# Optimization experiments

Measured on AMD Instinct MI355X. Metric: run time of the kernel, lower is better.

The kernel has to match this reference:

```python
import jax, jax.numpy as jnp
import numpy as np

N, E = 16384, 262144
D_NODE, D_EDGE, H = 256, 64, 8
EPS = 1e-5

def _lin(key, din, dout):
    kw, kb = jax.random.split(key)
    s = 1.0 / np.sqrt(din)
    W = jax.random.uniform(kw, (din, dout), jnp.float32, -s, s)
    b = jax.random.uniform(kb, (dout,), jnp.float32, -s, s)
    return W, b

def setup_inputs() -> dict:
    key = jax.random.key(0)
    ks = jax.random.split(key, 12)
    node_features = jax.random.normal(ks[0], (N, D_NODE), jnp.float32)
    edge_index = jax.random.randint(ks[1], (2, E), 0, N, jnp.int64)
    edge_features = jax.random.normal(ks[2], (E, D_EDGE), jnp.float32)
    Wn, bn = _lin(ks[3], D_NODE, D_NODE)
    Wq, bq = _lin(ks[4], D_NODE, D_NODE)
    Wk, bk = _lin(ks[5], D_NODE, D_NODE)
    Wv, bv = _lin(ks[6], D_NODE, D_NODE)
    We, be = _lin(ks[7], D_EDGE, D_NODE)
    A1, a1 = _lin(ks[8], 3 * D_NODE, D_NODE)
    A2, a2 = _lin(ks[9], D_NODE, H)
    gamma = jnp.ones((D_NODE,), jnp.float32)
    beta = jnp.zeros((D_NODE,), jnp.float32)
    return dict(node_features=node_features, edge_index=edge_index,
                edge_features=edge_features, Wn=Wn, bn=bn, Wq=Wq, bq=bq,
                Wk=Wk, bk=bk, Wv=Wv, bv=bv, We=We, be=be,
                A1=A1, a1=a1, A2=A2, a2=a2, gamma=gamma, beta=beta)

def _leaky(x):
    return jnp.where(x > 0, x, 0.2 * x)

def reference(node_features, edge_index, edge_features, Wn, bn, Wq, bq,
              Wk, bk, Wv, bv, We, be, A1, a1, A2, a2, gamma, beta):
    h = node_features @ Wn + bn                      # [N, d]
    q = node_features @ Wq + bq
    k = node_features @ Wk + bk
    v = node_features @ Wv + bv
    edge_h = edge_features @ We + be                 # [E, d]
    src, tgt = edge_index[0], edge_index[1]
    attn_in = jnp.concatenate([q[src], k[tgt], edge_h], axis=-1)  # [E, 3d]
    scores = _leaky(_leaky(attn_in @ A1 + a1) @ A2 + a2)          # [E, H]
    # softmax over ALL edges (dim=0) of head-mean, as in the original
    w = jax.nn.softmax(scores.mean(axis=-1), axis=0)              # [E]
    out = jnp.zeros_like(node_features).at[src].add(w[:, None] * v[tgt])
    x = h + out                                      # dropout is identity (eval)
    mu = x.mean(-1, keepdims=True)
    var = ((x - mu) ** 2).mean(-1, keepdims=True)
    return (x - mu) / jnp.sqrt(var + EPS) * gamma + beta
```

## Files before the change

kernel.cpp:

```cpp
#include <hip/hip_runtime.h>
#include <stdint.h>

#define NN 16384
#define EE 262144
#define DD 256

typedef float f32x4 __attribute__((ext_vector_type(4)));
typedef short s16x8 __attribute__((ext_vector_type(8)));
typedef unsigned short u16x4 __attribute__((ext_vector_type(4)));
typedef unsigned short u16x8 __attribute__((ext_vector_type(8)));

#define AS1 __attribute__((address_space(1)))
#define AS3 __attribute__((address_space(3)))

__device__ __forceinline__ float bf2f(unsigned short u) {
  union { unsigned int i; float f; } v; v.i = ((unsigned int)u) << 16; return v.f;
}
__device__ __forceinline__ unsigned short f2bf(float f) {
  union { float f; unsigned int i; } v; v.f = f;
  unsigned int r = v.i + 0x7fffu + ((v.i >> 16) & 1u);
  return (unsigned short)(r >> 16);
}
__device__ __forceinline__ float lrelu(float x) { return x > 0.f ? x : 0.2f * x; }

__device__ __forceinline__ int chanperm(int c) {
  int hi = c & ~63, loc = c & 63;
  int ct = loc >> 4, quad = (loc >> 2) & 3, r = loc & 3;
  return hi | (quad * 16 + ct * 4 + r);
}

__global__ __launch_bounds__(256) void prep_kernel(
    const float* __restrict__ Wn, const float* __restrict__ bn,
    const float* __restrict__ Wq, const float* __restrict__ bq,
    const float* __restrict__ Wk, const float* __restrict__ bk,
    const float* __restrict__ Wv, const float* __restrict__ bv,
    const float* __restrict__ We, const float* __restrict__ be,
    const float* __restrict__ A1, const float* __restrict__ a1,
    const float* __restrict__ A2,
    unsigned short* __restrict__ BcatT, float* __restrict__ bcat,
    unsigned short* __restrict__ WeaT, float* __restrict__ bcomb,
    float* __restrict__ A2p)
{
  const int b = blockIdx.x, t = threadIdx.x;
  if (b < 256) {
    float acc = 0.f;
    for (int j = 0; j < 256; ++j) acc += Wq[b * 256 + j] * A1[j * 256 + t];
    BcatT[(512 + t) * 256 + b] = f2bf(acc);
  } else if (b < 512) {
    int k = b - 256; float acc = 0.f;
    for (int j = 0; j < 256; ++j) acc += Wk[k * 256 + j] * A1[(256 + j) * 256 + t];
    BcatT[(768 + t) * 256 + k] = f2bf(acc);
  } else if (b < 576) {
    int k = b - 512; float acc = 0.f;
    for (int j = 0; j < 256; ++j) acc += We[k * 256 + j] * A1[(512 + j) * 256 + t];
    WeaT[chanperm(t) * 64 + k] = f2bf(acc);
  } else if (b == 576) {
    float acc = a1[t];
    for (int j = 0; j < 256; ++j) {
      acc += bq[j] * A1[j * 256 + t];
      acc += bk[j] * A1[(256 + j) * 256 + t];
      acc += be[j] * A1[(512 + j) * 256 + t];
    }
    bcomb[chanperm(t)] = acc;
  } else if (b < 705) {
    int b2 = b - 577;
    for (int rr = 0; rr < 4; ++rr) {
      int np = b2 * 4 + rr;
      float v = (np < 256) ? Wn[t * 256 + np] : Wv[t * 256 + (np - 256)];
      BcatT[np * 256 + t] = f2bf(v);
    }
  } else if (b == 705) {
    bcat[t] = bn[t];
    bcat[256 + t] = bv[t];
    bcat[512 + t] = 0.f;
    bcat[768 + t] = 0.f;
  } else {
    int m = chanperm(t);
    for (int j = 0; j < 8; ++j) A2p[m * 8 + j] = A2[t * 8 + j];
  }
}

__global__ __launch_bounds__(256) void conv_hist_kernel(
    const float* __restrict__ in, unsigned short* __restrict__ o,
    const int* __restrict__ eidx, int* __restrict__ deg)
{
  size_t i = (size_t)blockIdx.x * 256 + threadIdx.x;
  const f32x4* p = (const f32x4*)(in + i * 8);
  f32x4 a = p[0], b = p[1];
  u16x8 r = { f2bf(a[0]), f2bf(a[1]), f2bf(a[2]), f2bf(a[3]),
              f2bf(b[0]), f2bf(b[1]), f2bf(b[2]), f2bf(b[3]) };
  *(u16x8*)(o + i * 8) = r;
  if (blockIdx.x < EE / 256) {
    int e = blockIdx.x * 256 + threadIdx.x;
    atomicAdd(&deg[eidx[e]], 1);
  }
}

__global__ __launch_bounds__(256, 1) void node_gemm_kernel(
    const unsigned short* __restrict__ Abf,
    const unsigned short* __restrict__ BT,
    const float* __restrict__ bias,
    float* __restrict__ hout, unsigned short* __restrict__ vout,
    unsigned short* __restrict__ Qa, unsigned short* __restrict__ Ka)
{
  __shared__ __align__(16) unsigned short Al[128 * 64];
  __shared__ __align__(16) unsigned short Bl[128 * 64];
  const int t = threadIdx.x;
  const int wid = t >> 6, lane = t & 63;
  const int quad = lane >> 4, l15 = lane & 15;
  const int mblk = blockIdx.x & 127, nblk = blockIdx.x >> 7;
  const int m0 = mblk * 128, n0 = nblk * 128;
  const int mh = wid >> 1, nh = wid & 1;
  const int srow = lane >> 3, sslot = lane & 7;

  f32x4 acc[4][4];
  #pragma unroll
  for (int i = 0; i < 4; ++i)
    #pragma unroll
    for (int j = 0; j < 4; ++j) acc[i][j] = (f32x4){0.f, 0.f, 0.f, 0.f};

  for (int ks = 0; ks < 4; ++ks) {
    const int k0 = ks * 64;
    #pragma unroll
    for (int j = 0; j < 4; ++j) {
      int cj = wid * 4 + j;
      int row = cj * 8 + srow;
      const unsigned short* ga =
          Abf + (size_t)(m0 + row) * 256 + k0 + ((sslot ^ (row & 7)) * 8);
      __builtin_amdgcn_global_load_lds((AS1 const void*)ga,
                                       (AS3 void*)(Al + cj * 512), 16, 0, 0);
      const unsigned short* gb =
          BT + (size_t)(n0 + row) * 256 + k0 + ((sslot ^ (row & 7)) * 8);
      __builtin_amdgcn_global_load_lds((AS1 const void*)gb,
                                       (AS3 void*)(Bl + cj * 512), 16, 0, 0);
    }
    __syncthreads();
    s16x8 af[4][2], bfr[4][2];
    #pragma unroll
    for (int mt = 0; mt < 4; ++mt) {
      int row = mh * 64 + mt * 16 + l15;
      #pragma unroll
      for (int kk = 0; kk < 2; ++kk) {
        int s = (kk * 4 + quad) ^ (row & 7);
        af[mt][kk] = *(const s16x8*)(Al + row * 64 + s * 8);
      }
    }
    #pragma unroll
    for (int nt = 0; nt < 4; ++nt) {
      int row = nh * 64 + nt * 16 + l15;
      #pragma unroll
      for (int kk = 0; kk < 2; ++kk) {
        int s = (kk * 4 + quad) ^ (row & 7);
        bfr[nt][kk] = *(const s16x8*)(Bl + row * 64 + s * 8);
      }
    }
    #pragma unroll
    for (int mt = 0; mt < 4; ++mt)
      #pragma unroll
      for (int nt = 0; nt < 4; ++nt) {
        acc[mt][nt] = __builtin_amdgcn_mfma_f32_16x16x32_bf16(
            af[mt][0], bfr[nt][0], acc[mt][nt], 0, 0, 0);
        acc[mt][nt] = __builtin_amdgcn_mfma_f32_16x16x32_bf16(
            af[mt][1], bfr[nt][1], acc[mt][nt], 0, 0, 0);
      }
    __syncthreads();
  }

  #pragma unroll
  for (int nt = 0; nt < 4; ++nt) {
    int n = n0 + nh * 64 + nt * 16 + l15;
    float bb = bias[n];
    int seg = n >> 8;
    int ncol = n & 255;
    #pragma unroll
    for (int mt = 0; mt < 4; ++mt) {
      int m = m0 + mh * 64 + mt * 16 + quad * 4;
      f32x4 a = acc[mt][nt];
      #pragma unroll
      for (int r = 0; r < 4; ++r) {
        float val = a[r] + bb;
        size_t idx = (size_t)(m + r) * 256 + ncol;
        if (seg == 0) hout[idx] = val;
        else if (seg == 1) vout[idx] = f2bf(val);
        else if (seg == 2) Qa[idx] = f2bf(val);
        else Ka[idx] = f2bf(val);
      }
    }
  }
}

__global__ __launch_bounds__(256) void scan_kernel(
    const int* __restrict__ deg, int* __restrict__ startA, int* __restrict__ cursor)
{
  __shared__ int ls[256];
  const int t = threadIdx.x;
  int4 d[16];
  int s = 0;
  #pragma unroll
  for (int i = 0; i < 16; ++i) {
    d[i] = ((const int4*)deg)[t * 16 + i];
    s += d[i].x + d[i].y + d[i].z + d[i].w;
  }
  ls[t] = s;
  __syncthreads();
  for (int dd = 1; dd < 256; dd <<= 1) {
    int v = ls[t];
    if (t >= dd) v += ls[t - dd];
    __syncthreads();
    ls[t] = v;
    __syncthreads();
  }
  int run = ls[t] - s;
  #pragma unroll
  for (int i = 0; i < 16; ++i) {
    int4 o;
    o.x = run; run += d[i].x;
    o.y = run; run += d[i].y;
    o.z = run; run += d[i].z;
    o.w = run; run += d[i].w;
    ((int4*)startA)[t * 16 + i] = o;
    ((int4*)cursor)[t * 16 + i] = o;
  }
  if (t == 255) startA[NN] = run;
}

__global__ __launch_bounds__(256) void perm_kernel(
    const int* __restrict__ eidx, int* __restrict__ cursor,
    int* __restrict__ perm, int* __restrict__ srcp, int* __restrict__ tgtp)
{
  int e = blockIdx.x * 256 + threadIdx.x;
  int s = eidx[e], tg = eidx[EE + e];
  int pos = atomicAdd(&cursor[s], 1);
  perm[pos] = e;
  srcp[pos] = s;
  tgtp[pos] = tg;
}

__global__ __launch_bounds__(256, 4) void edge_scores_kernel(
    const int* __restrict__ perm, const int* __restrict__ srcp,
    const int* __restrict__ tgtp, const float* __restrict__ ef,
    const unsigned short* __restrict__ Qa, const unsigned short* __restrict__ Ka,
    const unsigned short* __restrict__ WeaT, const float* __restrict__ bcomb,
    const float* __restrict__ A2p, const float* __restrict__ a2g,
    float* __restrict__ Pp, float* __restrict__ Z)
{
  __shared__ __align__(16) unsigned short efl[64 * 64];
  __shared__ __align__(16) float A2l[256 * 12];
  __shared__ __align__(16) float pl[4 * 64 * 8];
  __shared__ __align__(16) float bcl[256];
  __shared__ int srcl[64], tgtl[64];
  const int t = threadIdx.x;
  const int wid = t >> 6, lane = t & 63, quad = lane >> 4, l15 = lane & 15;
  const int eb = blockIdx.x * 64;

  {
    const f32x4* sp = (const f32x4*)(A2p + t * 8);
    f32x4 x0 = sp[0], x1 = sp[1];
    *(f32x4*)&A2l[t * 12] = x0;
    *(f32x4*)&A2l[t * 12 + 4] = x1;
  }
  if (t < 64) srcl[t] = srcp[eb + t];
  else if (t < 128) tgtl[t - 64] = tgtp[eb + (t - 64)];
  else if (t < 192) ((f32x4*)bcl)[t - 128] = ((const f32x4*)bcomb)[t - 128];
  {
    int r = t >> 2, q4 = t & 3;
    int pe = perm[eb + r];
    const f32x4* sp = (const f32x4*)(ef + (size_t)pe * 64 + q4 * 16);
    f32x4 v0 = sp[0], v1 = sp[1], v2 = sp[2], v3 = sp[3];
    u16x8 w0 = { f2bf(v0[0]), f2bf(v0[1]), f2bf(v0[2]), f2bf(v0[3]),
                 f2bf(v1[0]), f2bf(v1[1]), f2bf(v1[2]), f2bf(v1[3]) };
    u16x8 w1 = { f2bf(v2[0]), f2bf(v2[1]), f2bf(v2[2]), f2bf(v2[3]),
                 f2bf(v3[0]), f2bf(v3[1]), f2bf(v3[2]), f2bf(v3[3]) };
    int s0_ = (2 * q4) ^ (r & 7), s1_ = (2 * q4 + 1) ^ (r & 7);
    *(u16x8*)&efl[r * 64 + s0_ * 8] = w0;
    *(u16x8*)&efl[r * 64 + s1_ * 8] = w1;
  }
  __syncthreads();

  f32x4 acc[4][4];
  {
    const int cb = wid * 64 + quad * 16;
    #pragma unroll
    for (int eo = 0; eo < 2; ++eo) {
      u16x8 q0[2], q1[2], k0[2], k1[2];
      #pragma unroll
      for (int x = 0; x < 2; ++x) {
        int e = (eo * 2 + x) * 16 + l15;
        const unsigned short* qr = Qa + (size_t)srcl[e] * 256 + cb;
        const unsigned short* kr = Ka + (size_t)tgtl[e] * 256 + cb;
        q0[x] = *(const u16x8*)qr; q1[x] = *(const u16x8*)(qr + 8);
        k0[x] = *(const u16x8*)kr; k1[x] = *(const u16x8*)(kr + 8);
      }
      #pragma unroll
      for (int x = 0; x < 2; ++x) {
        int et = eo * 2 + x;
        #pragma unroll
        for (int r = 0; r < 4; ++r) {
          acc[0][et][r] = bf2f(q0[x][r])     + bf2f(k0[x][r]);
          acc[1][et][r] = bf2f(q0[x][4 + r]) + bf2f(k0[x][4 + r]);
          acc[2][et][r] = bf2f(q1[x][r])     + bf2f(k1[x][r]);
          acc[3][et][r] = bf2f(q1[x][4 + r]) + bf2f(k1[x][4 + r]);
        }
      }
    }
  }

  {
    s16x8 af0[4], af1[4];
    #pragma unroll
    for (int ct = 0; ct < 4; ++ct) {
      int ch = wid * 64 + ct * 16 + l15;
      af0[ct] = *(const s16x8*)(WeaT + ch * 64 + quad * 8);
      af1[ct] = *(const s16x8*)(WeaT + ch * 64 + 32 + quad * 8);
    }
    #pragma unroll
    for (int et = 0; et < 4; ++et) {
      int e = et * 16 + l15;
      s16x8 b0 = *(const s16x8*)(efl + e * 64 + ((quad ^ (e & 7)) * 8));
      s16x8 b1 = *(const s16x8*)(efl + e * 64 + (((4 + quad) ^ (e & 7)) * 8));
      #pragma unroll
      for (int ct = 0; ct < 4; ++ct) {
        acc[ct][et] = __builtin_amdgcn_mfma_f32_16x16x32_bf16(af0[ct], b0, acc[ct][et], 0, 0, 0);
        acc[ct][et] = __builtin_amdgcn_mfma_f32_16x16x32_bf16(af1[ct], b1, acc[ct][et], 0, 0, 0);
      }
    }
  }

  float part[4][8];
  #pragma unroll
  for (int i = 0; i < 4; ++i)
    #pragma unroll
    for (int j = 0; j < 8; ++j) part[i][j] = 0.f;
  #pragma unroll
  for (int ct = 0; ct < 4; ++ct) {
    int chb = wid * 64 + ct * 16 + quad * 4;
    f32x4 bc = *(const f32x4*)&bcl[chb];
    #pragma unroll
    for (int r = 0; r < 4; ++r) {
      f32x4 w0 = *(const f32x4*)&A2l[(chb + r) * 12];
      f32x4 w1 = *(const f32x4*)&A2l[(chb + r) * 12 + 4];
      #pragma unroll
      for (int et = 0; et < 4; ++et) {
        float m = lrelu(acc[ct][et][r] + bc[r]);
        part[et][0] += m * w0[0]; part[et][1] += m * w0[1];
        part[et][2] += m * w0[2]; part[et][3] += m * w0[3];
        part[et][4] += m * w1[0]; part[et][5] += m * w1[1];
        part[et][6] += m * w1[2]; part[et][7] += m * w1[3];
      }
    }
  }
  #pragma unroll
  for (int et = 0; et < 4; ++et)
    #pragma unroll
    for (int hh = 0; hh < 8; ++hh) {
      part[et][hh] += __shfl_xor(part[et][hh], 16);
      part[et][hh] += __shfl_xor(part[et][hh], 32);
    }
  if (quad == 0) {
    #pragma unroll
    for (int et = 0; et < 4; ++et) {
      f32x4 p0 = { part[et][0], part[et][1], part[et][2], part[et][3] };
      f32x4 p1 = { part[et][4], part[et][5], part[et][6], part[et][7] };
      int e = et * 16 + l15;
      *(f32x4*)&pl[(wid * 64 + e) * 8] = p0;
      *(f32x4*)&pl[(wid * 64 + e) * 8 + 4] = p1;
    }
  }
  __syncthreads();
  if (t < 64) {
    f32x4 t0 = {0.f, 0.f, 0.f, 0.f}, t1 = {0.f, 0.f, 0.f, 0.f};
    #pragma unroll
    for (int w2 = 0; w2 < 4; ++w2) {
      t0 += *(const f32x4*)&pl[(w2 * 64 + t) * 8];
      t1 += *(const f32x4*)&pl[(w2 * 64 + t) * 8 + 4];
    }
    float sacc = 0.f;
    #pragma unroll
    for (int j = 0; j < 4; ++j) {
      sacc += lrelu(t0[j] + a2g[j]);
      sacc += lrelu(t1[j] + a2g[4 + j]);
    }
    float p = __expf(sacc * 0.125f);
    Pp[eb + t] = p;
    #pragma unroll
    for (int d = 1; d < 64; d <<= 1) p += __shfl_xor(p, d);
    if (t == 0) atomicAdd(Z, p);
  }
}

__global__ __launch_bounds__(256) void scatter_ln_kernel(
    const int* __restrict__ startA, const float* __restrict__ Pp,
    const float* __restrict__ Zp, const int* __restrict__ tgtp,
    const unsigned short* __restrict__ vbuf, const float* __restrict__ hbuf,
    const float* __restrict__ gamma, const float* __restrict__ beta,
    float* __restrict__ out)
{
  const int wid = threadIdx.x >> 6, lane = threadIdx.x & 63;
  const int n = blockIdx.x * 4 + wid;
  const float invZ = 1.f / Zp[0];
  const int s0 = startA[n], s1 = startA[n + 1];
  float a0 = 0.f, a1_ = 0.f, a2_ = 0.f, a3_ = 0.f;
  int i = s0;
  for (; i + 1 < s1; i += 2) {
    float w0 = Pp[i], w1 = Pp[i + 1];
    int t0 = tgtp[i], t1 = tgtp[i + 1];
    u16x4 v0 = *(const u16x4*)(vbuf + (size_t)t0 * 256 + lane * 4);
    u16x4 v1 = *(const u16x4*)(vbuf + (size_t)t1 * 256 + lane * 4);
    w0 *= invZ; w1 *= invZ;
    a0 += w0 * bf2f(v0[0]) + w1 * bf2f(v1[0]);
    a1_ += w0 * bf2f(v0[1]) + w1 * bf2f(v1[1]);
    a2_ += w0 * bf2f(v0[2]) + w1 * bf2f(v1[2]);
    a3_ += w0 * bf2f(v0[3]) + w1 * bf2f(v1[3]);
  }
  if (i < s1) {
    float w0 = Pp[i] * invZ;
    int t0 = tgtp[i];
    u16x4 v0 = *(const u16x4*)(vbuf + (size_t)t0 * 256 + lane * 4);
    a0 += w0 * bf2f(v0[0]); a1_ += w0 * bf2f(v0[1]);
    a2_ += w0 * bf2f(v0[2]); a3_ += w0 * bf2f(v0[3]);
  }
  f32x4 hv = *(const f32x4*)(hbuf + (size_t)n * 256 + lane * 4);
  float x0 = hv[0] + a0, x1 = hv[1] + a1_, x2 = hv[2] + a2_, x3 = hv[3] + a3_;
  float sum = x0 + x1 + x2 + x3;
  float sq = x0 * x0 + x1 * x1 + x2 * x2 + x3 * x3;
  #pragma unroll
  for (int d = 1; d < 64; d <<= 1) { sum += __shfl_xor(sum, d); sq += __shfl_xor(sq, d); }
  float mu = sum * (1.f / 256.f);
  float var = sq * (1.f / 256.f) - mu * mu;
  float rstd = rsqrtf(var + 1e-5f);
  f32x4 g = *(const f32x4*)(gamma + lane * 4);
  f32x4 b = *(const f32x4*)(beta + lane * 4);
  f32x4 o;
  o[0] = (x0 - mu) * rstd * g[0] + b[0];
  o[1] = (x1 - mu) * rstd * g[1] + b[1];
  o[2] = (x2 - mu) * rstd * g[2] + b[2];
  o[3] = (x3 - mu) * rstd * g[3] + b[3];
  *(f32x4*)(out + (size_t)n * 256 + lane * 4) = o;
}

extern "C" void kernel_launch(void* const* d_in, const int* in_sizes, int n_in,
                              void* d_out, int out_size, void* d_ws, size_t ws_size,
                              hipStream_t stream)
{
  (void)in_sizes; (void)n_in; (void)out_size; (void)ws_size;
  const float* nf    = (const float*)d_in[0];
  const int*   eidx  = (const int*)  d_in[1];
  const float* ef    = (const float*)d_in[2];
  const float* Wn    = (const float*)d_in[3];
  const float* bn    = (const float*)d_in[4];
  const float* Wq    = (const float*)d_in[5];
  const float* bq    = (const float*)d_in[6];
  const float* Wk    = (const float*)d_in[7];
  const float* bk    = (const float*)d_in[8];
  const float* Wv    = (const float*)d_in[9];
  const float* bv    = (const float*)d_in[10];
  const float* We    = (const float*)d_in[11];
  const float* be    = (const float*)d_in[12];
  const float* A1    = (const float*)d_in[13];
  const float* a1    = (const float*)d_in[14];
  const float* A2    = (const float*)d_in[15];
  const float* a2    = (const float*)d_in[16];
  const float* gamma = (const float*)d_in[17];
  const float* beta  = (const float*)d_in[18];
  float* out = (float*)d_out;

  char* ws = (char*)d_ws;
  size_t off = 0;
  auto take = [&](size_t bytes) {
    size_t r = off; off += (bytes + 255) & ~(size_t)255; return r;
  };
  float* Z       = (float*)(ws + take(16));
  int*   deg     = (int*)  (ws + take((size_t)NN * 4));
  int*   startA  = (int*)  (ws + take((size_t)(NN + 1) * 4));
  int*   cursor  = (int*)  (ws + take((size_t)NN * 4));
  int*   perm    = (int*)  (ws + take((size_t)EE * 4));
  int*   srcp    = (int*)  (ws + take((size_t)EE * 4));
  int*   tgtp    = (int*)  (ws + take((size_t)EE * 4));
  float* Pp      = (float*)(ws + take((size_t)EE * 4));
  float* hbuf    = (float*)(ws + take((size_t)NN * DD * 4));
  unsigned short* vbuf  = (unsigned short*)(ws + take((size_t)NN * DD * 2));
  unsigned short* QaB   = (unsigned short*)(ws + take((size_t)NN * DD * 2));
  unsigned short* KaB   = (unsigned short*)(ws + take((size_t)NN * DD * 2));
  unsigned short* BcatT = (unsigned short*)(ws + take((size_t)1024 * 256 * 2));
  float* bcat    = (float*)(ws + take(1024 * 4));
  unsigned short* WeaT  = (unsigned short*)(ws + take((size_t)256 * 64 * 2));
  float* bcomb   = (float*)(ws + take(256 * 4));
  float* A2p     = (float*)(ws + take(256 * 8 * 4));
  unsigned short* nfb   = (unsigned short*)(ws + take((size_t)NN * DD * 2));

  hipMemsetAsync(d_ws, 0, 256 + (size_t)NN * 4, stream);

  prep_kernel<<<707, 256, 0, stream>>>(Wn, bn, Wq, bq, Wk, bk, Wv, bv,
                                       We, be, A1, a1, A2,
                                       BcatT, bcat, WeaT, bcomb, A2p);
  conv_hist_kernel<<<(NN * DD / 8) / 256, 256, 0, stream>>>(nf, nfb, eidx, deg);
  node_gemm_kernel<<<1024, 256, 0, stream>>>(nfb, BcatT, bcat, hbuf, vbuf, QaB, KaB);
  scan_kernel<<<1, 256, 0, stream>>>(deg, startA, cursor);
  perm_kernel<<<EE / 256, 256, 0, stream>>>(eidx, cursor, perm, srcp, tgtp);
  edge_scores_kernel<<<EE / 64, 256, 0, stream>>>(perm, srcp, tgtp, ef, QaB, KaB,
                                                  WeaT, bcomb, A2p, a2, Pp, Z);
  scatter_ln_kernel<<<NN / 4, 256, 0, stream>>>(startA, Pp, Z, tgtp, vbuf, hbuf,
                                                gamma, beta, out);
}
```

Baseline: 347.9 us.

## Merge launches, persist edge-score blocks with prefetch, bf16 h buffer, sharded Z

Cuts the launch chain from seven kernels to five. The histogram moves into the prep kernel, the scan into the conversion kernel, and the edge permutation into the GEMM kernel as extra blocks. The edge-score kernel now handles four 64-edge tiles per block, keeps the We weights resident in registers and prefetches the next tile's indices and edge features. It also reduces Z into 64 partial slots instead of one global atomic. The h buffer is stored as bf16 to halve its traffic, and the scatter loop is unrolled by 4. The bf16 h adds rounding error to the residual path.

```diff
diff --git a/kernel.cpp b/kernel.cpp
--- a/kernel.cpp
+++ b/kernel.cpp
@@ -25,21 +25,21 @@
 
 __device__ __forceinline__ int chanperm(int c) {
   int hi = c & ~63, loc = c & 63;
-  int ct = loc >> 4, quad = (loc >> 2) & 3, r = loc & 3;
-  return hi | (quad * 16 + ct * 4 + r);
-}
-
-__global__ __launch_bounds__(256) void prep_kernel(
+  int ct = loc >> 4, quad = (loc >> 2) & 3, rr = loc & 3;
+  return hi | (quad * 16 + ct * 4 + rr);
+}
+
+__global__ __launch_bounds__(256) void prep_hist_kernel(
     const float* __restrict__ Wn, const float* __restrict__ bn,
     const float* __restrict__ Wq, const float* __restrict__ bq,
     const float* __restrict__ Wk, const float* __restrict__ bk,
     const float* __restrict__ Wv, const float* __restrict__ bv,
     const float* __restrict__ We, const float* __restrict__ be,
     const float* __restrict__ A1, const float* __restrict__ a1,
-    const float* __restrict__ A2,
+    const float* __restrict__ A2, const int* __restrict__ eidx,
     unsigned short* __restrict__ BcatT, float* __restrict__ bcat,
     unsigned short* __restrict__ WeaT, float* __restrict__ bcomb,
-    float* __restrict__ A2p)
+    float* __restrict__ A2p, int* __restrict__ deg)
 {
   const int b = blockIdx.x, t = threadIdx.x;
   if (b < 256) {
@@ -74,41 +74,86 @@
     bcat[256 + t] = bv[t];
     bcat[512 + t] = 0.f;
     bcat[768 + t] = 0.f;
-  } else {
+  } else if (b == 706) {
     int m = chanperm(t);
     for (int j = 0; j < 8; ++j) A2p[m * 8 + j] = A2[t * 8 + j];
-  }
-}
-
-__global__ __launch_bounds__(256) void conv_hist_kernel(
+  } else {
+    int e = (b - 707) * 256 + t;
+    atomicAdd(&deg[eidx[e]], 1);
+  }
+}
+
+__global__ __launch_bounds__(256) void conv_scan_kernel(
     const float* __restrict__ in, unsigned short* __restrict__ o,
-    const int* __restrict__ eidx, int* __restrict__ deg)
+    const int* __restrict__ deg, int* __restrict__ startA,
+    int* __restrict__ cursor)
 {
-  size_t i = (size_t)blockIdx.x * 256 + threadIdx.x;
-  const f32x4* p = (const f32x4*)(in + i * 8);
-  f32x4 a = p[0], b = p[1];
-  u16x8 r = { f2bf(a[0]), f2bf(a[1]), f2bf(a[2]), f2bf(a[3]),
-              f2bf(b[0]), f2bf(b[1]), f2bf(b[2]), f2bf(b[3]) };
-  *(u16x8*)(o + i * 8) = r;
-  if (blockIdx.x < EE / 256) {
-    int e = blockIdx.x * 256 + threadIdx.x;
-    atomicAdd(&deg[eidx[e]], 1);
-  }
-}
-
-__global__ __launch_bounds__(256, 1) void node_gemm_kernel(
+  const int t = threadIdx.x;
+  if (blockIdx.x < 2048) {
+    size_t i = (size_t)blockIdx.x * 256 + t;
+    const f32x4* p = (const f32x4*)(in + i * 8);
+    f32x4 a = p[0], b = p[1];
+    u16x8 r = { f2bf(a[0]), f2bf(a[1]), f2bf(a[2]), f2bf(a[3]),
+                f2bf(b[0]), f2bf(b[1]), f2bf(b[2]), f2bf(b[3]) };
+    *(u16x8*)(o + i * 8) = r;
+    return;
+  }
+  __shared__ int ls[256];
+  int4 d[16];
+  int s = 0;
+  #pragma unroll
+  for (int i = 0; i < 16; ++i) {
+    d[i] = ((const int4*)deg)[t * 16 + i];
+    s += d[i].x + d[i].y + d[i].z + d[i].w;
+  }
+  ls[t] = s;
+  __syncthreads();
+  for (int dd = 1; dd < 256; dd <<= 1) {
+    int v = ls[t];
+    if (t >= dd) v += ls[t - dd];
+    __syncthreads();
+    ls[t] = v;
+    __syncthreads();
+  }
+  int run = ls[t] - s;
+  #pragma unroll
+  for (int i = 0; i < 16; ++i) {
+    int4 ov;
+    ov.x = run; run += d[i].x;
+    ov.y = run; run += d[i].y;
+    ov.z = run; run += d[i].z;
+    ov.w = run; run += d[i].w;
+    ((int4*)startA)[t * 16 + i] = ov;
+    ((int4*)cursor)[t * 16 + i] = ov;
+  }
+  if (t == 255) startA[NN] = run;
+}
+
+__global__ __launch_bounds__(256, 1) void gemm_perm_kernel(
     const unsigned short* __restrict__ Abf,
     const unsigned short* __restrict__ BT,
     const float* __restrict__ bias,
-    float* __restrict__ hout, unsigned short* __restrict__ vout,
-    unsigned short* __restrict__ Qa, unsigned short* __restrict__ Ka)
+    unsigned short* __restrict__ hout, unsigned short* __restrict__ vout,
+    unsigned short* __restrict__ Qa, unsigned short* __restrict__ Ka,
+    const int* __restrict__ eidx, int* __restrict__ cursor,
+    int* __restrict__ perm, int* __restrict__ srcp, int* __restrict__ tgtp)
 {
+  const int t = threadIdx.x;
+  if (blockIdx.x < 1024) {
+    int e = blockIdx.x * 256 + t;
+    int s = eidx[e], tg = eidx[EE + e];
+    int pos = atomicAdd(&cursor[s], 1);
+    perm[pos] = e;
+    srcp[pos] = s;
+    tgtp[pos] = tg;
+    return;
+  }
   __shared__ __align__(16) unsigned short Al[128 * 64];
   __shared__ __align__(16) unsigned short Bl[128 * 64];
-  const int t = threadIdx.x;
+  const int b2 = blockIdx.x - 1024;
   const int wid = t >> 6, lane = t & 63;
   const int quad = lane >> 4, l15 = lane & 15;
-  const int mblk = blockIdx.x & 127, nblk = blockIdx.x >> 7;
+  const int mblk = b2 & 127, nblk = b2 >> 7;
   const int m0 = mblk * 128, n0 = nblk * 128;
   const int mh = wid >> 1, nh = wid & 1;
   const int srow = lane >> 3, sslot = lane & 7;
@@ -180,60 +225,13 @@
       for (int r = 0; r < 4; ++r) {
         float val = a[r] + bb;
         size_t idx = (size_t)(m + r) * 256 + ncol;
-        if (seg == 0) hout[idx] = val;
+        if (seg == 0) hout[idx] = f2bf(val);
         else if (seg == 1) vout[idx] = f2bf(val);
         else if (seg == 2) Qa[idx] = f2bf(val);
         else Ka[idx] = f2bf(val);
       }
     }
   }
-}
-
-__global__ __launch_bounds__(256) void scan_kernel(
-    const int* __restrict__ deg, int* __restrict__ startA, int* __restrict__ cursor)
-{
-  __shared__ int ls[256];
-  const int t = threadIdx.x;
-  int4 d[16];
-  int s = 0;
-  #pragma unroll
-  for (int i = 0; i < 16; ++i) {
-    d[i] = ((const int4*)deg)[t * 16 + i];
-    s += d[i].x + d[i].y + d[i].z + d[i].w;
-  }
-  ls[t] = s;
-  __syncthreads();
-  for (int dd = 1; dd < 256; dd <<= 1) {
-    int v = ls[t];
-    if (t >= dd) v += ls[t - dd];
-    __syncthreads();
-    ls[t] = v;
-    __syncthreads();
-  }
-  int run = ls[t] - s;
-  #pragma unroll
-  for (int i = 0; i < 16; ++i) {
-    int4 o;
-    o.x = run; run += d[i].x;
-    o.y = run; run += d[i].y;
-    o.z = run; run += d[i].z;
-    o.w = run; run += d[i].w;
-    ((int4*)startA)[t * 16 + i] = o;
-    ((int4*)cursor)[t * 16 + i] = o;
-  }
-  if (t == 255) startA[NN] = run;
-}
-
-__global__ __launch_bounds__(256) void perm_kernel(
-    const int* __restrict__ eidx, int* __restrict__ cursor,
-    int* __restrict__ perm, int* __restrict__ srcp, int* __restrict__ tgtp)
-{
-  int e = blockIdx.x * 256 + threadIdx.x;
-  int s = eidx[e], tg = eidx[EE + e];
-  int pos = atomicAdd(&cursor[s], 1);
-  perm[pos] = e;
-  srcp[pos] = s;
-  tgtp[pos] = tg;
 }
 
 __global__ __launch_bounds__(256, 4) void edge_scores_kernel(
@@ -242,7 +240,7 @@
     const unsigned short* __restrict__ Qa, const unsigned short* __restrict__ Ka,
     const unsigned short* __restrict__ WeaT, const float* __restrict__ bcomb,
     const float* __restrict__ A2p, const float* __restrict__ a2g,
-    float* __restrict__ Pp, float* __restrict__ Z)
+    float* __restrict__ Pp, float* __restrict__ Zpart)
 {
   __shared__ __align__(16) unsigned short efl[64 * 64];
   __shared__ __align__(16) float A2l[256 * 12];
@@ -251,7 +249,8 @@
   __shared__ int srcl[64], tgtl[64];
   const int t = threadIdx.x;
   const int wid = t >> 6, lane = t & 63, quad = lane >> 4, l15 = lane & 15;
-  const int eb = blockIdx.x * 64;
+  const int base = blockIdx.x * 256;
+  const int r = t >> 2, q4 = t & 3;
 
   {
     const f32x4* sp = (const f32x4*)(A2p + t * 8);
@@ -259,59 +258,77 @@
     *(f32x4*)&A2l[t * 12] = x0;
     *(f32x4*)&A2l[t * 12 + 4] = x1;
   }
-  if (t < 64) srcl[t] = srcp[eb + t];
-  else if (t < 128) tgtl[t - 64] = tgtp[eb + (t - 64)];
-  else if (t < 192) ((f32x4*)bcl)[t - 128] = ((const f32x4*)bcomb)[t - 128];
+  if (t < 64) ((f32x4*)bcl)[t] = ((const f32x4*)bcomb)[t];
+
+  s16x8 af0[4], af1[4];
+  #pragma unroll
+  for (int ct = 0; ct < 4; ++ct) {
+    int ch = wid * 64 + ct * 16 + l15;
+    af0[ct] = *(const s16x8*)(WeaT + ch * 64 + quad * 8);
+    af1[ct] = *(const s16x8*)(WeaT + ch * 64 + 32 + quad * 8);
+  }
+  const f32x4 a20 = *(const f32x4*)a2g;
+  const f32x4 a21 = *(const f32x4*)(a2g + 4);
+
+  int pe = perm[base + r];
+  int rs = (t < 128) ? ((t < 64) ? srcp[base + t] : tgtp[base + t - 64]) : 0;
+  f32x4 v0, v1, v2, v3;
   {
-    int r = t >> 2, q4 = t & 3;
-    int pe = perm[eb + r];
     const f32x4* sp = (const f32x4*)(ef + (size_t)pe * 64 + q4 * 16);
-    f32x4 v0 = sp[0], v1 = sp[1], v2 = sp[2], v3 = sp[3];
-    u16x8 w0 = { f2bf(v0[0]), f2bf(v0[1]), f2bf(v0[2]), f2bf(v0[3]),
-                 f2bf(v1[0]), f2bf(v1[1]), f2bf(v1[2]), f2bf(v1[3]) };
-    u16x8 w1 = { f2bf(v2[0]), f2bf(v2[1]), f2bf(v2[2]), f2bf(v2[3]),
-                 f2bf(v3[0]), f2bf(v3[1]), f2bf(v3[2]), f2bf(v3[3]) };
-    int s0_ = (2 * q4) ^ (r & 7), s1_ = (2 * q4 + 1) ^ (r & 7);
-    *(u16x8*)&efl[r * 64 + s0_ * 8] = w0;
-    *(u16x8*)&efl[r * 64 + s1_ * 8] = w1;
-  }
-  __syncthreads();
-
-  f32x4 acc[4][4];
-  {
-    const int cb = wid * 64 + quad * 16;
-    #pragma unroll
-    for (int eo = 0; eo < 2; ++eo) {
-      u16x8 q0[2], q1[2], k0[2], k1[2];
-      #pragma unroll
-      for (int x = 0; x < 2; ++x) {
-        int e = (eo * 2 + x) * 16 + l15;
-        const unsigned short* qr = Qa + (size_t)srcl[e] * 256 + cb;
-        const unsigned short* kr = Ka + (size_t)tgtl[e] * 256 + cb;
-        q0[x] = *(const u16x8*)qr; q1[x] = *(const u16x8*)(qr + 8);
-        k0[x] = *(const u16x8*)kr; k1[x] = *(const u16x8*)(kr + 8);
-      }
-      #pragma unroll
-      for (int x = 0; x < 2; ++x) {
-        int et = eo * 2 + x;
+    v0 = sp[0]; v1 = sp[1]; v2 = sp[2]; v3 = sp[3];
+  }
+  int pe_n = perm[base + 64 + r];
+
+  float zacc = 0.f;
+
+  #pragma unroll
+  for (int k = 0; k < 4; ++k) {
+    const int eb = base + k * 64;
+    {
+      u16x8 w0 = { f2bf(v0[0]), f2bf(v0[1]), f2bf(v0[2]), f2bf(v0[3]),
+                   f2bf(v1[0]), f2bf(v1[1]), f2bf(v1[2]), f2bf(v1[3]) };
+      u16x8 w1 = { f2bf(v2[0]), f2bf(v2[1]), f2bf(v2[2]), f2bf(v2[3]),
+                   f2bf(v3[0]), f2bf(v3[1]), f2bf(v3[2]), f2bf(v3[3]) };
+      int s0_ = (2 * q4) ^ (r & 7), s1_ = (2 * q4 + 1) ^ (r & 7);
+      *(u16x8*)&efl[r * 64 + s0_ * 8] = w0;
+      *(u16x8*)&efl[r * 64 + s1_ * 8] = w1;
+    }
+    if (t < 64) srcl[t] = rs;
+    else if (t < 128) tgtl[t - 64] = rs;
+    if (k < 3) {
+      rs = (t < 128) ? ((t < 64) ? srcp[eb + 64 + t] : tgtp[eb + t]) : 0;
+      const f32x4* sp = (const f32x4*)(ef + (size_t)pe_n * 64 + q4 * 16);
+      v0 = sp[0]; v1 = sp[1]; v2 = sp[2]; v3 = sp[3];
+      if (k < 2) pe_n = perm[eb + 128 + r];
+    }
+    __syncthreads();
+
+    f32x4 acc[4][4];
+    {
+      const int cb = wid * 64 + quad * 16;
+      #pragma unroll
+      for (int eo = 0; eo < 2; ++eo) {
+        u16x8 q0[2], q1[2], k0[2], k1[2];
         #pragma unroll
-        for (int r = 0; r < 4; ++r) {
-          acc[0][et][r] = bf2f(q0[x][r])     + bf2f(k0[x][r]);
-          acc[1][et][r] = bf2f(q0[x][4 + r]) + bf2f(k0[x][4 + r]);
-          acc[2][et][r] = bf2f(q1[x][r])     + bf2f(k1[x][r]);
-          acc[3][et][r] = bf2f(q1[x][4 + r]) + bf2f(k1[x][4 + r]);
+        for (int x = 0; x < 2; ++x) {
+          int e = (eo * 2 + x) * 16 + l15;
+          const unsigned short* qr = Qa + (size_t)srcl[e] * 256 + cb;
+          const unsigned short* kr = Ka + (size_t)tgtl[e] * 256 + cb;
+          q0[x] = *(const u16x8*)qr; q1[x] = *(const u16x8*)(qr + 8);
+          k0[x] = *(const u16x8*)kr; k1[x] = *(const u16x8*)(kr + 8);
         }
-      }
-    }
-  }
-
-  {
-    s16x8 af0[4], af1[4];
-    #pragma unroll
-    for (int ct = 0; ct < 4; ++ct) {
-      int ch = wid * 64 + ct * 16 + l15;
-      af0[ct] = *(const s16x8*)(WeaT + ch * 64 + quad * 8);
-      af1[ct] = *(const s16x8*)(WeaT + ch * 64 + 32 + quad * 8);
+        #pragma unroll
+        for (int x = 0; x < 2; ++x) {
+          int et = eo * 2 + x;
+          #pragma unroll
+          for (int rr = 0; rr < 4; ++rr) {
+            acc[0][et][rr] = bf2f(q0[x][rr])     + bf2f(k0[x][rr]);
+            acc[1][et][rr] = bf2f(q0[x][4 + rr]) + bf2f(k0[x][4 + rr]);
+            acc[2][et][rr] = bf2f(q1[x][rr])     + bf2f(k1[x][rr]);
+            acc[3][et][rr] = bf2f(q1[x][4 + rr]) + bf2f(k1[x][4 + rr]);
+          }
+        }
+      }
     }
     #pragma unroll
     for (int et = 0; et < 4; ++et) {
@@ -324,103 +341,109 @@
         acc[ct][et] = __builtin_amdgcn_mfma_f32_16x16x32_bf16(af1[ct], b1, acc[ct][et], 0, 0, 0);
       }
     }
-  }
-
-  float part[4][8];
-  #pragma unroll
-  for (int i = 0; i < 4; ++i)
-    #pragma unroll
-    for (int j = 0; j < 8; ++j) part[i][j] = 0.f;
-  #pragma unroll
-  for (int ct = 0; ct < 4; ++ct) {
-    int chb = wid * 64 + ct * 16 + quad * 4;
-    f32x4 bc = *(const f32x4*)&bcl[chb];
-    #pragma unroll
-    for (int r = 0; r < 4; ++r) {
-      f32x4 w0 = *(const f32x4*)&A2l[(chb + r) * 12];
-      f32x4 w1 = *(const f32x4*)&A2l[(chb + r) * 12 + 4];
+    float part[4][8];
+    #pragma unroll
+    for (int i = 0; i < 4; ++i)
+      #pragma unroll
+      for (int j = 0; j < 8; ++j) part[i][j] = 0.f;
+    #pragma unroll
+    for (int ct = 0; ct < 4; ++ct) {
+      int chb = wid * 64 + ct * 16 + quad * 4;
+      f32x4 bc = *(const f32x4*)&bcl[chb];
+      #pragma unroll
+      for (int rr = 0; rr < 4; ++rr) {
+        f32x4 w0 = *(const f32x4*)&A2l[(chb + rr) * 12];
+        f32x4 w1 = *(const f32x4*)&A2l[(chb + rr) * 12 + 4];
+        #pragma unroll
+        for (int et = 0; et < 4; ++et) {
+          float m = lrelu(acc[ct][et][rr] + bc[rr]);
+          part[et][0] += m * w0[0]; part[et][1] += m * w0[1];
+          part[et][2] += m * w0[2]; part[et][3] += m * w0[3];
+          part[et][4] += m * w1[0]; part[et][5] += m * w1[1];
+          part[et][6] += m * w1[2]; part[et][7] += m * w1[3];
+        }
+      }
+    }
+    #pragma unroll
+    for (int et = 0; et < 4; ++et)
+      #pragma unroll
+      for (int hh = 0; hh < 8; ++hh) {
+        part[et][hh] += __shfl_xor(part[et][hh], 16);
+        part[et][hh] += __shfl_xor(part[et][hh], 32);
+      }
+    if (quad == 0) {
       #pragma unroll
       for (int et = 0; et < 4; ++et) {
-        float m = lrelu(acc[ct][et][r] + bc[r]);
-        part[et][0] += m * w0[0]; part[et][1] += m * w0[1];
-        part[et][2] += m * w0[2]; part[et][3] += m * w0[3];
-        part[et][4] += m * w1[0]; part[et][5] += m * w1[1];
-        part[et][6] += m * w1[2]; part[et][7] += m * w1[3];
-      }
-    }
-  }
-  #pragma unroll
-  for (int et = 0; et < 4; ++et)
-    #pragma unroll
-    for (int hh = 0; hh < 8; ++hh) {
-      part[et][hh] += __shfl_xor(part[et][hh], 16);
-      part[et][hh] += __shfl_xor(part[et][hh], 32);
-    }
-  if (quad == 0) {
-    #pragma unroll
-    for (int et = 0; et < 4; ++et) {
-      f32x4 p0 = { part[et][0], part[et][1], part[et][2], part[et][3] };
-      f32x4 p1 = { part[et][4], part[et][5], part[et][6], part[et][7] };
-      int e = et * 16 + l15;
-      *(f32x4*)&pl[(wid * 64 + e) * 8] = p0;
-      *(f32x4*)&pl[(wid * 64 + e) * 8 + 4] = p1;
-    }
-  }
-  __syncthreads();
-  if (t < 64) {
-    f32x4 t0 = {0.f, 0.f, 0.f, 0.f}, t1 = {0.f, 0.f, 0.f, 0.f};
-    #pragma unroll
-    for (int w2 = 0; w2 < 4; ++w2) {
-      t0 += *(const f32x4*)&pl[(w2 * 64 + t) * 8];
-      t1 += *(const f32x4*)&pl[(w2 * 64 + t) * 8 + 4];
-    }
-    float sacc = 0.f;
-    #pragma unroll
-    for (int j = 0; j < 4; ++j) {
-      sacc += lrelu(t0[j] + a2g[j]);
-      sacc += lrelu(t1[j] + a2g[4 + j]);
-    }
-    float p = __expf(sacc * 0.125f);
-    Pp[eb + t] = p;
-    #pragma unroll
-    for (int d = 1; d < 64; d <<= 1) p += __shfl_xor(p, d);
-    if (t == 0) atomicAdd(Z, p);
-  }
+        f32x4 p0 = { part[et][0], part[et][1], part[et][2], part[et][3] };
+        f32x4 p1 = { part[et][4], part[et][5], part[et][6], part[et][7] };
+        int e = et * 16 + l15;
+        *(f32x4*)&pl[(wid * 64 + e) * 8] = p0;
+        *(f32x4*)&pl[(wid * 64 + e) * 8 + 4] = p1;
+      }
+    }
+    __syncthreads();
+    if (t < 64) {
+      f32x4 t0 = {0.f, 0.f, 0.f, 0.f}, t1 = {0.f, 0.f, 0.f, 0.f};
+      #pragma unroll
+      for (int w2 = 0; w2 < 4; ++w2) {
+        t0 += *(const f32x4*)&pl[(w2 * 64 + t) * 8];
+        t1 += *(const f32x4*)&pl[(w2 * 64 + t) * 8 + 4];
+      }
+      float sacc = 0.f;
+      #pragma unroll
+      for (int j = 0; j < 4; ++j) {
+        sacc += lrelu(t0[j] + a20[j]);
+        sacc += lrelu(t1[j] + a21[j]);
+      }
+      float p = __expf(sacc * 0.125f);
+      Pp[eb + t] = p;
+      #pragma unroll
+      for (int d = 1; d < 64; d <<= 1) p += __shfl_xor(p, d);
+      zacc += p;
+    }
+  }
+  if (t == 0) atomicAdd(&Zpart[blockIdx.x & 63], zacc);
 }
 
 __global__ __launch_bounds__(256) void scatter_ln_kernel(
     const int* __restrict__ startA, const float* __restrict__ Pp,
-    const float* __restrict__ Zp, const int* __restrict__ tgtp,
-    const unsigned short* __restrict__ vbuf, const float* __restrict__ hbuf,
+    const float* __restrict__ Zpart, const int* __restrict__ tgtp,
+    const unsigned short* __restrict__ vbuf, const unsigned short* __restrict__ hbuf,
     const float* __restrict__ gamma, const float* __restrict__ beta,
     float* __restrict__ out)
 {
   const int wid = threadIdx.x >> 6, lane = threadIdx.x & 63;
   const int n = blockIdx.x * 4 + wid;
-  const float invZ = 1.f / Zp[0];
+  float zv = Zpart[lane];
+  #pragma unroll
+  for (int d = 1; d < 64; d <<= 1) zv += __shfl_xor(zv, d);
+  const float invZ = 1.f / zv;
   const int s0 = startA[n], s1 = startA[n + 1];
   float a0 = 0.f, a1_ = 0.f, a2_ = 0.f, a3_ = 0.f;
   int i = s0;
-  for (; i + 1 < s1; i += 2) {
-    float w0 = Pp[i], w1 = Pp[i + 1];
-    int t0 = tgtp[i], t1 = tgtp[i + 1];
-    u16x4 v0 = *(const u16x4*)(vbuf + (size_t)t0 * 256 + lane * 4);
-    u16x4 v1 = *(const u16x4*)(vbuf + (size_t)t1 * 256 + lane * 4);
-    w0 *= invZ; w1 *= invZ;
-    a0 += w0 * bf2f(v0[0]) + w1 * bf2f(v1[0]);
-    a1_ += w0 * bf2f(v0[1]) + w1 * bf2f(v1[1]);
-    a2_ += w0 * bf2f(v0[2]) + w1 * bf2f(v1[2]);
-    a3_ += w0 * bf2f(v0[3]) + w1 * bf2f(v1[3]);
-  }
-  if (i < s1) {
+  for (; i + 3 < s1; i += 4) {
+    float w0 = Pp[i], w1 = Pp[i + 1], w2 = Pp[i + 2], w3 = Pp[i + 3];
+    int t0 = tgtp[i], t1 = tgtp[i + 1], t2 = tgtp[i + 2], t3 = tgtp[i + 3];
+    u16x4 e0 = *(const u16x4*)(vbuf + (size_t)t0 * 256 + lane * 4);
+    u16x4 e1 = *(const u16x4*)(vbuf + (size_t)t1 * 256 + lane * 4);
+    u16x4 e2 = *(const u16x4*)(vbuf + (size_t)t2 * 256 + lane * 4);
+    u16x4 e3 = *(const u16x4*)(vbuf + (size_t)t3 * 256 + lane * 4);
+    w0 *= invZ; w1 *= invZ; w2 *= invZ; w3 *= invZ;
+    a0 += w0 * bf2f(e0[0]) + w1 * bf2f(e1[0]) + w2 * bf2f(e2[0]) + w3 * bf2f(e3[0]);
+    a1_ += w0 * bf2f(e0[1]) + w1 * bf2f(e1[1]) + w2 * bf2f(e2[1]) + w3 * bf2f(e3[1]);
+    a2_ += w0 * bf2f(e0[2]) + w1 * bf2f(e1[2]) + w2 * bf2f(e2[2]) + w3 * bf2f(e3[2]);
+    a3_ += w0 * bf2f(e0[3]) + w1 * bf2f(e1[3]) + w2 * bf2f(e2[3]) + w3 * bf2f(e3[3]);
+  }
+  for (; i < s1; ++i) {
     float w0 = Pp[i] * invZ;
     int t0 = tgtp[i];
-    u16x4 v0 = *(const u16x4*)(vbuf + (size_t)t0 * 256 + lane * 4);
-    a0 += w0 * bf2f(v0[0]); a1_ += w0 * bf2f(v0[1]);
-    a2_ += w0 * bf2f(v0[2]); a3_ += w0 * bf2f(v0[3]);
-  }
-  f32x4 hv = *(const f32x4*)(hbuf + (size_t)n * 256 + lane * 4);
-  float x0 = hv[0] + a0, x1 = hv[1] + a1_, x2 = hv[2] + a2_, x3 = hv[3] + a3_;
+    u16x4 e0 = *(const u16x4*)(vbuf + (size_t)t0 * 256 + lane * 4);
+    a0 += w0 * bf2f(e0[0]); a1_ += w0 * bf2f(e0[1]);
+    a2_ += w0 * bf2f(e0[2]); a3_ += w0 * bf2f(e0[3]);
+  }
+  u16x4 hv = *(const u16x4*)(hbuf + (size_t)n * 256 + lane * 4);
+  float x0 = bf2f(hv[0]) + a0, x1 = bf2f(hv[1]) + a1_;
+  float x2 = bf2f(hv[2]) + a2_, x3 = bf2f(hv[3]) + a3_;
   float sum = x0 + x1 + x2 + x3;
   float sq = x0 * x0 + x1 * x1 + x2 * x2 + x3 * x3;
   #pragma unroll
@@ -469,7 +492,7 @@
   auto take = [&](size_t bytes) {
     size_t r = off; off += (bytes + 255) & ~(size_t)255; return r;
   };
-  float* Z       = (float*)(ws + take(16));
+  float* Zpart   = (float*)(ws + take(256));
   int*   deg     = (int*)  (ws + take((size_t)NN * 4));
   int*   startA  = (int*)  (ws + take((size_t)(NN + 1) * 4));
   int*   cursor  = (int*)  (ws + take((size_t)NN * 4));
@@ -477,7 +500,7 @@
   int*   srcp    = (int*)  (ws + take((size_t)EE * 4));
   int*   tgtp    = (int*)  (ws + take((size_t)EE * 4));
   float* Pp      = (float*)(ws + take((size_t)EE * 4));
-  float* hbuf    = (float*)(ws + take((size_t)NN * DD * 4));
+  unsigned short* hbuf  = (unsigned short*)(ws + take((size_t)NN * DD * 2));
   unsigned short* vbuf  = (unsigned short*)(ws + take((size_t)NN * DD * 2));
   unsigned short* QaB   = (unsigned short*)(ws + take((size_t)NN * DD * 2));
   unsigned short* KaB   = (unsigned short*)(ws + take((size_t)NN * DD * 2));
@@ -490,15 +513,15 @@
 
   hipMemsetAsync(d_ws, 0, 256 + (size_t)NN * 4, stream);
 
-  prep_kernel<<<707, 256, 0, stream>>>(Wn, bn, Wq, bq, Wk, bk, Wv, bv,
-                                       We, be, A1, a1, A2,
-                                       BcatT, bcat, WeaT, bcomb, A2p);
-  conv_hist_kernel<<<(NN * DD / 8) / 256, 256, 0, stream>>>(nf, nfb, eidx, deg);
-  node_gemm_kernel<<<1024, 256, 0, stream>>>(nfb, BcatT, bcat, hbuf, vbuf, QaB, KaB);
-  scan_kernel<<<1, 256, 0, stream>>>(deg, startA, cursor);
-  perm_kernel<<<EE / 256, 256, 0, stream>>>(eidx, cursor, perm, srcp, tgtp);
-  edge_scores_kernel<<<EE / 64, 256, 0, stream>>>(perm, srcp, tgtp, ef, QaB, KaB,
-                                                  WeaT, bcomb, A2p, a2, Pp, Z);
-  scatter_ln_kernel<<<NN / 4, 256, 0, stream>>>(startA, Pp, Z, tgtp, vbuf, hbuf,
-                                                gamma, beta, out);
-}
+  prep_hist_kernel<<<1731, 256, 0, stream>>>(Wn, bn, Wq, bq, Wk, bk, Wv, bv,
+                                             We, be, A1, a1, A2, eidx,
+                                             BcatT, bcat, WeaT, bcomb, A2p, deg);
+  conv_scan_kernel<<<2049, 256, 0, stream>>>(nf, nfb, deg, startA, cursor);
+  gemm_perm_kernel<<<2048, 256, 0, stream>>>(nfb, BcatT, bcat, hbuf, vbuf,
+                                             QaB, KaB, eidx, cursor,
+                                             perm, srcp, tgtp);
+  edge_scores_kernel<<<1024, 256, 0, stream>>>(perm, srcp, tgtp, ef, QaB, KaB,
+                                               WeaT, bcomb, A2p, a2, Pp, Zpart);
+  scatter_ln_kernel<<<NN / 4, 256, 0, stream>>>(startA, Pp, Zpart, tgtp,
+                                                vbuf, hbuf, gamma, beta, out);
+}
```

After: 350.5 us. About the same (+0.8%).
